# Performance work log

Measured on AMD Instinct MI355X. Metric: run time of the kernel, lower is better.

## Reference

```python
import jax, jax.numpy as jnp
import numpy as np

NUM_HEADS = 16
HEAD_DIM = 64
ROPE_THETA = 10000.0


def _rope_cos_sin(n, dtype):
    # Llama RoPE: inv_freq over even dims, emb = concat(freqs, freqs)
    inv_freq = 1.0 / (ROPE_THETA ** (jnp.arange(0, HEAD_DIM, 2, dtype=jnp.float32) / HEAD_DIM))
    freqs = jnp.arange(n, dtype=jnp.float32)[:, None] * inv_freq[None, :]  # [N, D/2]
    emb = jnp.concatenate([freqs, freqs], axis=-1)  # [N, D]
    return jnp.cos(emb).astype(dtype), jnp.sin(emb).astype(dtype)


def _rotate_half(x):
    x1, x2 = jnp.split(x, 2, axis=-1)
    return jnp.concatenate([-x2, x1], axis=-1)


def setup_inputs() -> dict:
    key = jax.random.key(0)
    ks = jax.random.split(key, 5)
    B, N, H = 2, 2048, 1024
    feature = jax.random.normal(ks[0], (B, N, H), dtype=jnp.float32)
    attention_mask = jnp.ones((B, N), dtype=jnp.int32)
    scale = 0.02
    Wq = jax.random.normal(ks[1], (H, H), dtype=jnp.float32) * scale
    Wk = jax.random.normal(ks[2], (H, H), dtype=jnp.float32) * scale
    Wv = jax.random.normal(ks[3], (H, H), dtype=jnp.float32) * scale
    Wo = jax.random.normal(ks[4], (H, H), dtype=jnp.float32) * scale
    return {"feature": feature, "attention_mask": attention_mask,
            "Wq": Wq, "Wk": Wk, "Wv": Wv, "Wo": Wo}


def reference(feature, attention_mask, Wq, Wk, Wv, Wo):
    B, N, H = feature.shape
    h, d = NUM_HEADS, HEAD_DIM
    scale = d ** -0.5

    def proj(x, W):  # nn.Linear(bias=False): x @ W.T
        y = jnp.einsum('bnh,oh->bno', x, W)
        return y.reshape(B, N, h, d).transpose(0, 2, 1, 3)  # [B,h,N,d]

    q, k, v = proj(feature, Wq), proj(feature, Wk), proj(feature, Wv)

    cos, sin = _rope_cos_sin(N, feature.dtype)  # [N, d]
    cos = cos[None, None]  # [1,1,N,d]
    sin = sin[None, None]
    q = q * cos + _rotate_half(q) * sin
    k = k * cos + _rotate_half(k) * sin

    scores = jnp.einsum('bhqd,bhkd->bhqk', q, k) * scale  # [B,h,N,N]
    mask = (attention_mask != 0)[:, None, None, :]  # [B,1,1,N]
    scores = jnp.where(mask, scores, jnp.float32(-jnp.inf).astype(scores.dtype))
    weights = jax.nn.softmax(scores, axis=-1)

    out = jnp.einsum('bhqk,bhkd->bhqd', weights, v)  # [B,h,N,d]
    out = out.transpose(0, 2, 1, 3).reshape(B, N, H)
    return jnp.einsum('bnh,oh->bno', out, Wo)
```

## Files before the change

### kernel.cpp

```cpp
#include <hip/hip_runtime.h>
#include <hip/hip_bf16.h>

typedef __attribute__((ext_vector_type(4))) float f32x4;
typedef __attribute__((ext_vector_type(8))) short s16x8;
typedef __attribute__((ext_vector_type(4))) short s16x4;

#define BB 2
#define NN 2048
#define HH 1024
#define NHEAD 16
#define HDIM 64

__device__ __forceinline__ short f2bf(float f) {
  union { float f; unsigned u; } v; v.f = f;
  unsigned r = v.u + 0x7fffu + ((v.u >> 16) & 1u);
  return (short)(r >> 16);
}

__device__ __forceinline__ f32x4 zf4() { f32x4 z; z[0]=0.f; z[1]=0.f; z[2]=0.f; z[3]=0.f; return z; }

__device__ __forceinline__ f32x4 mfma16(s16x8 a, s16x8 b, f32x4 c) {
  return __builtin_amdgcn_mfma_f32_16x16x32_bf16(a, b, c, 0, 0, 0);
}

__device__ __forceinline__ s16x4 cvt4(f32x4 v) {
  s16x4 o; o[0]=f2bf(v[0]); o[1]=f2bf(v[1]); o[2]=f2bf(v[2]); o[3]=f2bf(v[3]); return o;
}

__device__ __forceinline__ float vexp2(float x) {
  float r; asm("v_exp_f32 %0, %1" : "=v"(r) : "v"(x)); return r;
}

__device__ __forceinline__ float vrcp(float x) {
  float r; asm("v_rcp_f32 %0, %1" : "=v"(r) : "v"(x)); return r;
}

__device__ __forceinline__ unsigned cvtpk_bf16(float lo, float hi) {
  unsigned r; asm("v_cvt_pk_bf16_f32 %0, %1, %2" : "=v"(r) : "v"(lo), "v"(hi)); return r;
}

__global__ __launch_bounds__(256) void prep_kernel(
    const float* __restrict__ feat, const int* __restrict__ mask,
    const float* __restrict__ wq, const float* __restrict__ wk,
    const float* __restrict__ wv, const float* __restrict__ wo,
    short* __restrict__ fbf, short* __restrict__ wqb, short* __restrict__ wkb,
    short* __restrict__ wvb, short* __restrict__ wob,
    float* __restrict__ cosb, float* __restrict__ sinb,
    float* __restrict__ mbias, int* __restrict__ mseg) {
  const int tid = blockIdx.x * blockDim.x + threadIdx.x;
  const int nth = gridDim.x * blockDim.x;
  const int NF4 = BB*NN*HH/4;
  for (int i = tid; i < NF4; i += nth)
    ((s16x4*)fbf)[i] = cvt4(((const f32x4*)feat)[i]);
  const int NW4 = HH*HH/4;
  for (int i = tid; i < NW4; i += nth) {
    ((s16x4*)wqb)[i] = cvt4(((const f32x4*)wq)[i]);
    ((s16x4*)wkb)[i] = cvt4(((const f32x4*)wk)[i]);
    ((s16x4*)wvb)[i] = cvt4(((const f32x4*)wv)[i]);
    ((s16x4*)wob)[i] = cvt4(((const f32x4*)wo)[i]);
  }
  for (int i = tid; i < NN*32; i += nth) {
    int pos = i >> 5, f = i & 31;
    float inv = __expf(-(float)f * 0.28782313662425572f);
    float ang = (float)pos * inv;
    float s, c;
    sincosf(ang, &s, &c);
    cosb[i] = c; sinb[i] = s;
  }
  for (int i = tid; i < BB*NN; i += nth)
    mbias[i] = mask[i] ? 0.f : -1.0e30f;
  for (int i = tid; i < BB*(NN/64); i += nth) {
    int bb = i / (NN/64), sg = i % (NN/64);
    int any = 0;
    for (int j = 0; j < 64; ++j) any |= (mask[bb*NN + sg*64 + j] == 0);
    mseg[i] = any;
  }
}

__device__ __forceinline__ void gemm128_core(
    const short* __restrict__ A, const short* __restrict__ W,
    int bm, int bn, short* smem, f32x4 acc[4][4]) {
  const int tid = threadIdx.x;
  const int lane = tid & 63, wid = tid >> 6;
  const int wr = wid >> 1, wc = wid & 1;
  const int g = lane >> 4, lr = lane & 15;
  short* At = smem;
  short* Bt = smem + 5120;
#pragma unroll
  for (int i = 0; i < 4; ++i)
#pragma unroll
    for (int j = 0; j < 4; ++j) acc[i][j] = zf4();

  const int srow = tid >> 2;
  const int scol = (tid & 3) * 8;
  const short* Aptr = A + (size_t)(bm*128 + srow) * HH + scol;
  const short* Wptr = W + (size_t)(bn*128 + srow) * HH + scol;

  s16x8 ra0 = *(const s16x8*)(Aptr);
  s16x8 ra1 = *(const s16x8*)(Aptr + 64*HH);
  s16x8 rb0 = *(const s16x8*)(Wptr);
  s16x8 rb1 = *(const s16x8*)(Wptr + 64*HH);

  const int NT = HH / 32;
  for (int t = 0; t < NT; ++t) {
    *(s16x8*)&At[srow*40 + scol]      = ra0;
    *(s16x8*)&At[(srow+64)*40 + scol] = ra1;
    *(s16x8*)&Bt[srow*40 + scol]      = rb0;
    *(s16x8*)&Bt[(srow+64)*40 + scol] = rb1;
    __syncthreads();
    if (t + 1 < NT) {
      const short* ap = Aptr + (t+1)*32;
      const short* wp = Wptr + (t+1)*32;
      ra0 = *(const s16x8*)(ap);
      ra1 = *(const s16x8*)(ap + 64*HH);
      rb0 = *(const s16x8*)(wp);
      rb1 = *(const s16x8*)(wp + 64*HH);
    }
    s16x8 af[4], bf[4];
#pragma unroll
    for (int mf = 0; mf < 4; ++mf)
      af[mf] = *(const s16x8*)&At[(wr*64 + mf*16 + lr)*40 + g*8];
#pragma unroll
    for (int nf = 0; nf < 4; ++nf)
      bf[nf] = *(const s16x8*)&Bt[(wc*64 + nf*16 + lr)*40 + g*8];
#pragma unroll
    for (int mf = 0; mf < 4; ++mf)
#pragma unroll
      for (int nf = 0; nf < 4; ++nf)
        acc[mf][nf] = mfma16(af[mf], bf[nf], acc[mf][nf]);
    __syncthreads();
  }
}

__global__ __launch_bounds__(256) void qkv_kernel(
    const short* __restrict__ fbf, const short* __restrict__ wqb,
    const short* __restrict__ wkb, const short* __restrict__ wvb,
    const float* __restrict__ cosb, const float* __restrict__ sinb,
    short* __restrict__ qb, short* __restrict__ kb, short* __restrict__ vtb) {
  __shared__ short smem[18432];
  const int bm = blockIdx.y, bn = blockIdx.x, z = blockIdx.z;
  const short* W = (z == 0) ? wqb : ((z == 1) ? wkb : wvb);
  f32x4 acc[4][4];
  gemm128_core(fbf, W, bm, bn, smem, acc);

  const int tid = threadIdx.x, lane = tid & 63, wid = tid >> 6;
  const int wr = wid >> 1, wc = wid & 1, g = lane >> 4, lr = lane & 15;
  const int head = bn*2 + wc;
  const int m0 = bm*128 + wr*64;
  const int b = m0 / NN;

  if (z < 2) {
    short* dst = (z == 0) ? qb : kb;
    const float scale = (z == 0) ? 0.18033688011112042f : 1.0f;
#pragma unroll
    for (int mf = 0; mf < 4; ++mf) {
#pragma unroll
      for (int r = 0; r < 4; ++r) {
        int m = m0 + mf*16 + g*4 + r;
        int n = m & (NN - 1);
        float c0 = cosb[n*32 + lr],      s0 = sinb[n*32 + lr];
        float c1 = cosb[n*32 + 16 + lr], s1 = sinb[n*32 + 16 + lr];
        float v0 = acc[mf][0][r], v1 = acc[mf][1][r];
        float v2 = acc[mf][2][r], v3 = acc[mf][3][r];
        float o0 = (v0*c0 - v2*s0) * scale;
        float o1 = (v1*c1 - v3*s1) * scale;
        float o2 = (v2*c0 + v0*s0) * scale;
        float o3 = (v3*c1 + v1*s1) * scale;
        size_t base = ((size_t)(b*NHEAD + head)*NN + n)*HDIM;
        dst[base +  0 + lr] = f2bf(o0);
        dst[base + 16 + lr] = f2bf(o1);
        dst[base + 32 + lr] = f2bf(o2);
        dst[base + 48 + lr] = f2bf(o3);
      }
    }
  } else {
    __syncthreads();
    short* tp = smem + wid*4608;
#pragma unroll
    for (int mf = 0; mf < 4; ++mf)
#pragma unroll
      for (int nf = 0; nf < 4; ++nf)
#pragma unroll
        for (int r = 0; r < 4; ++r)
          tp[(nf*16 + lr)*72 + mf*16 + g*4 + r] = f2bf(acc[mf][nf][r]);
    __syncthreads();
    const int nbase = m0 & (NN - 1);
    size_t vbase = ((size_t)(b*NHEAD + head)*HDIM)*NN;
#pragma unroll
    for (int it = 0; it < 8; ++it) {
      int j  = it*8 + (lane >> 3);
      int ns = (lane & 7)*8;
      s16x8 vv = *(const s16x8*)&tp[j*72 + ns];
      *(s16x8*)&vtb[vbase + (size_t)j*NN + nbase + ns] = vv;
    }
  }
}

__global__ __launch_bounds__(256) void attn_kernel(
    const short* __restrict__ qb, const short* __restrict__ kb,
    const short* __restrict__ vtb, const float* __restrict__ mbias,
    const int* __restrict__ mseg,
    short* __restrict__ attnb) {
  __shared__ short Kt[64*72];
  __shared__ short Vt[64*72];
  __shared__ __align__(16) unsigned Pd[4][16*36];
  const int tid = threadIdx.x, lane = tid & 63, wid = tid >> 6;
  const int g = lane >> 4, lr = lane & 15;
  const int bh = blockIdx.y; const int b = bh >> 4;
  const int q0 = blockIdx.x*64 + wid*16;

  const short* qp = qb + ((size_t)bh*NN + q0 + lr)*HDIM + g*8;
  s16x8 qf0 = *(const s16x8*)(qp);
  s16x8 qf1 = *(const s16x8*)(qp + 32);

  f32x4 acc[4];
#pragma unroll
  for (int i = 0; i < 4; ++i) acc[i] = zf4();
  float mrun = -3.0e38f, lsum = 0.f;

  const int sr = tid >> 2;
  const int sc = (tid & 3) * 16;
  const short* kp = kb + (size_t)bh*NN*HDIM + (size_t)sr*HDIM + sc;
  const short* vp = vtb + ((size_t)bh*HDIM + sr)*NN + sc;
  const float* mb = mbias + b*NN;
  const int* msp = mseg + b*(NN/64);

  s16x8 kr0 = *(const s16x8*)(kp);
  s16x8 kr1 = *(const s16x8*)(kp + 8);
  s16x8 vr0 = *(const s16x8*)(vp);
  s16x8 vr1 = *(const s16x8*)(vp + 8);

  for (int k0 = 0; k0 < NN; k0 += 64) {
    *(s16x8*)&Kt[sr*72 + sc]     = kr0;
    *(s16x8*)&Kt[sr*72 + sc + 8] = kr1;
    *(s16x8*)&Vt[sr*72 + sc]     = vr0;
    *(s16x8*)&Vt[sr*72 + sc + 8] = vr1;
    __syncthreads();
    if (k0 + 64 < NN) {
      kp += 64*HDIM; vp += 64;
      kr0 = *(const s16x8*)(kp);
      kr1 = *(const s16x8*)(kp + 8);
      vr0 = *(const s16x8*)(vp);
      vr1 = *(const s16x8*)(vp + 8);
    }

    f32x4 s[4];
    __builtin_amdgcn_s_setprio(1);
#pragma unroll
    for (int kg = 0; kg < 4; ++kg) {
      s16x8 ka0 = *(const s16x8*)&Kt[(kg*16 + lr)*72 + g*8];
      s16x8 ka1 = *(const s16x8*)&Kt[(kg*16 + lr)*72 + 32 + g*8];
      s[kg] = mfma16(ka1, qf1, mfma16(ka0, qf0, zf4()));
    }
    __builtin_amdgcn_s_setprio(0);

    if (msp[k0 >> 6]) {
#pragma unroll
      for (int kg = 0; kg < 4; ++kg) {
        f32x4 bi = *(const f32x4*)&mb[k0 + kg*16 + g*4];
#pragma unroll
        for (int r = 0; r < 4; ++r) s[kg][r] += bi[r];
      }
    }

    float m0a = fmaxf(fmaxf(s[0][0], s[0][1]), fmaxf(s[0][2], s[0][3]));
    float m1a = fmaxf(fmaxf(s[1][0], s[1][1]), fmaxf(s[1][2], s[1][3]));
    float m2a = fmaxf(fmaxf(s[2][0], s[2][1]), fmaxf(s[2][2], s[2][3]));
    float m3a = fmaxf(fmaxf(s[3][0], s[3][1]), fmaxf(s[3][2], s[3][3]));
    float rmax = fmaxf(fmaxf(m0a, m1a), fmaxf(m2a, m3a));
    rmax = fmaxf(rmax, __shfl_xor(rmax, 16));
    rmax = fmaxf(rmax, __shfl_xor(rmax, 32));

    if (__any(rmax > mrun + 8.f)) {
      float mnew = fmaxf(mrun, rmax);
      float al = vexp2(mrun - mnew);
      mrun = mnew;
      lsum *= al;
      float alr[4];
#pragma unroll
      for (int r = 0; r < 4; ++r)
        alr[r] = __shfl(al, (lane & 48) | (g*4 + r));
#pragma unroll
      for (int db = 0; db < 4; ++db)
#pragma unroll
        for (int r = 0; r < 4; ++r) acc[db][r] *= alr[r];
    }

#pragma unroll
    for (int kg = 0; kg < 4; ++kg) {
      float p0 = vexp2(s[kg][0] - mrun);
      float p1 = vexp2(s[kg][1] - mrun);
      float p2 = vexp2(s[kg][2] - mrun);
      float p3 = vexp2(s[kg][3] - mrun);
      lsum += (p0 + p1) + (p2 + p3);
      unsigned* prow = &Pd[wid][lr*36 + kg*8 + g*2];
      prow[0] = cvtpk_bf16(p0, p1);
      prow[1] = cvtpk_bf16(p2, p3);
    }

    s16x8 pa0 = *(const s16x8*)&Pd[wid][lr*36 + g*4];
    s16x8 pa1 = *(const s16x8*)&Pd[wid][lr*36 + 16 + g*4];
    __builtin_amdgcn_s_setprio(1);
#pragma unroll
    for (int db = 0; db < 4; ++db) {
      s16x8 vb0 = *(const s16x8*)&Vt[(db*16 + lr)*72 + g*8];
      s16x8 vb1 = *(const s16x8*)&Vt[(db*16 + lr)*72 + 32 + g*8];
      acc[db] = mfma16(pa0, vb0, acc[db]);
      acc[db] = mfma16(pa1, vb1, acc[db]);
    }
    __builtin_amdgcn_s_setprio(0);
    __syncthreads();
  }

  lsum += __shfl_xor(lsum, 16);
  lsum += __shfl_xor(lsum, 32);
  float inv = vrcp(lsum);
  float invr[4];
#pragma unroll
  for (int r = 0; r < 4; ++r)
    invr[r] = __shfl(inv, (lane & 48) | (g*4 + r));
#pragma unroll
  for (int r = 0; r < 4; ++r) {
    size_t row = (size_t)(b*NN + q0 + g*4 + r);
#pragma unroll
    for (int db = 0; db < 4; ++db)
      attnb[row*HH + (bh & 15)*64 + db*16 + lr] = f2bf(acc[db][r]*invr[r]);
  }
}

__global__ __launch_bounds__(256) void outproj_kernel(
    const short* __restrict__ attnb, const short* __restrict__ wob,
    float* __restrict__ out) {
  __shared__ short smem[10240];
  const int bm = blockIdx.y, bn = blockIdx.x;
  f32x4 acc[4][4];
  gemm128_core(attnb, wob, bm, bn, smem, acc);
  const int tid = threadIdx.x, lane = tid & 63, wid = tid >> 6;
  const int wr = wid >> 1, wc = wid & 1, g = lane >> 4, lr = lane & 15;
  const int m0 = bm*128 + wr*64;
  const int c0 = bn*128 + wc*64;
#pragma unroll
  for (int mf = 0; mf < 4; ++mf)
#pragma unroll
    for (int r = 0; r < 4; ++r) {
      int m = m0 + mf*16 + g*4 + r;
      float* po = out + (size_t)m*HH + c0;
#pragma unroll
      for (int nf = 0; nf < 4; ++nf)
        po[nf*16 + lr] = acc[mf][nf][r];
    }
}

extern "C" void kernel_launch(void* const* d_in, const int* in_sizes, int n_in,
                              void* d_out, int out_size, void* d_ws, size_t ws_size,
                              hipStream_t stream) {
  const float* feat = (const float*)d_in[0];
  const int*   mask = (const int*)d_in[1];
  const float* wq   = (const float*)d_in[2];
  const float* wk   = (const float*)d_in[3];
  const float* wv   = (const float*)d_in[4];
  const float* wo   = (const float*)d_in[5];
  float* out = (float*)d_out;

  char* ws = (char*)d_ws;
  size_t off = 0;
  short* fbf = (short*)(ws + off); off += (size_t)BB*NN*HH*2;
  short* wqb = (short*)(ws + off); off += (size_t)HH*HH*2;
  short* wkb = (short*)(ws + off); off += (size_t)HH*HH*2;
  short* wvb = (short*)(ws + off); off += (size_t)HH*HH*2;
  short* wob = (short*)(ws + off); off += (size_t)HH*HH*2;
  float* cosb = (float*)(ws + off); off += (size_t)NN*32*4;
  float* sinb = (float*)(ws + off); off += (size_t)NN*32*4;
  float* mbias = (float*)(ws + off); off += (size_t)BB*NN*4;
  int* msegb = (int*)(ws + off); off += (size_t)BB*(NN/64)*4;
  short* qbuf = (short*)(ws + off); off += (size_t)BB*NN*HH*2;
  short* kbuf = (short*)(ws + off); off += (size_t)BB*NN*HH*2;
  short* vtbuf = (short*)(ws + off); off += (size_t)BB*NN*HH*2;
  short* attnb = (short*)(ws + off); off += (size_t)BB*NN*HH*2;

  prep_kernel<<<1024, 256, 0, stream>>>(feat, mask, wq, wk, wv, wo,
                                        fbf, wqb, wkb, wvb, wob, cosb, sinb,
                                        mbias, msegb);
  qkv_kernel<<<dim3(HH/128, BB*NN/128, 3), 256, 0, stream>>>(
      fbf, wqb, wkb, wvb, cosb, sinb, qbuf, kbuf, vtbuf);
  attn_kernel<<<dim3(NN/64, BB*NHEAD), 256, 0, stream>>>(
      qbuf, kbuf, vtbuf, mbias, msegb, attnb);
  outproj_kernel<<<dim3(HH/128, BB*NN/128), 256, 0, stream>>>(attnb, wob, out);
}
```

Baseline: 141.2 us.

## Load K/V fragments directly from global memory and remap blocks for L2 locality

The attention kernel no longer stages K and V tiles through shared memory with block-wide barriers. Each wave now loads its MFMA operand fragments for K and V straight from global memory, which removes the LDS writes and both __syncthreads per iteration. The grid is flattened and remapped so that consecutive blocks interleave heads, which is meant to spread work across XCDs while keeping each head's K/V reuse in cache. Each of the four waves now reads the full K/V tile on its own, so global and L2 traffic goes up, and the software prefetch of the next tile is dropped, which may expose load latency.

```diff
diff --git a/kernel.cpp b/kernel.cpp
--- a/kernel.cpp
+++ b/kernel.cpp
@@ -196,18 +196,19 @@
   }
 }
 
-__global__ __launch_bounds__(256) void attn_kernel(
+__global__ __launch_bounds__(256, 4) void attn_kernel(
     const short* __restrict__ qb, const short* __restrict__ kb,
     const short* __restrict__ vtb, const float* __restrict__ mbias,
     const int* __restrict__ mseg,
     short* __restrict__ attnb) {
-  __shared__ short Kt[64*72];
-  __shared__ short Vt[64*72];
   __shared__ __align__(16) unsigned Pd[4][16*36];
   const int tid = threadIdx.x, lane = tid & 63, wid = tid >> 6;
   const int g = lane >> 4, lr = lane & 15;
-  const int bh = blockIdx.y; const int b = bh >> 4;
-  const int q0 = blockIdx.x*64 + wid*16;
+  const int w = blockIdx.x;
+  const int bh = (w & 7) * 4 + ((w >> 3) >> 5);
+  const int qt = (w >> 3) & 31;
+  const int b = bh >> 4;
+  const int q0 = qt*64 + wid*16;
 
   const short* qp = qb + ((size_t)bh*NN + q0 + lr)*HDIM + g*8;
   s16x8 qf0 = *(const s16x8*)(qp);
@@ -218,40 +219,32 @@
   for (int i = 0; i < 4; ++i) acc[i] = zf4();
   float mrun = -3.0e38f, lsum = 0.f;
 
-  const int sr = tid >> 2;
-  const int sc = (tid & 3) * 16;
-  const short* kp = kb + (size_t)bh*NN*HDIM + (size_t)sr*HDIM + sc;
-  const short* vp = vtb + ((size_t)bh*HDIM + sr)*NN + sc;
+  const short* kbase = kb + (size_t)bh*NN*HDIM + (size_t)lr*HDIM + g*8;
+  const short* vbase = vtb + ((size_t)bh*HDIM + lr)*NN + g*8;
   const float* mb = mbias + b*NN;
   const int* msp = mseg + b*(NN/64);
 
-  s16x8 kr0 = *(const s16x8*)(kp);
-  s16x8 kr1 = *(const s16x8*)(kp + 8);
-  s16x8 vr0 = *(const s16x8*)(vp);
-  s16x8 vr1 = *(const s16x8*)(vp + 8);
-
+#pragma unroll 1
   for (int k0 = 0; k0 < NN; k0 += 64) {
-    *(s16x8*)&Kt[sr*72 + sc]     = kr0;
-    *(s16x8*)&Kt[sr*72 + sc + 8] = kr1;
-    *(s16x8*)&Vt[sr*72 + sc]     = vr0;
-    *(s16x8*)&Vt[sr*72 + sc + 8] = vr1;
-    __syncthreads();
-    if (k0 + 64 < NN) {
-      kp += 64*HDIM; vp += 64;
-      kr0 = *(const s16x8*)(kp);
-      kr1 = *(const s16x8*)(kp + 8);
-      vr0 = *(const s16x8*)(vp);
-      vr1 = *(const s16x8*)(vp + 8);
+    const short* kp = kbase + (size_t)k0*HDIM;
+    s16x8 kf[8];
+#pragma unroll
+    for (int kg = 0; kg < 4; ++kg) {
+      kf[kg*2]   = *(const s16x8*)(kp + kg*16*HDIM);
+      kf[kg*2+1] = *(const s16x8*)(kp + kg*16*HDIM + 32);
+    }
+    s16x8 vv[8];
+#pragma unroll
+    for (int db = 0; db < 4; ++db) {
+      vv[db*2]   = *(const s16x8*)(vbase + (size_t)db*16*NN + k0);
+      vv[db*2+1] = *(const s16x8*)(vbase + (size_t)db*16*NN + k0 + 32);
     }
 
     f32x4 s[4];
     __builtin_amdgcn_s_setprio(1);
 #pragma unroll
-    for (int kg = 0; kg < 4; ++kg) {
-      s16x8 ka0 = *(const s16x8*)&Kt[(kg*16 + lr)*72 + g*8];
-      s16x8 ka1 = *(const s16x8*)&Kt[(kg*16 + lr)*72 + 32 + g*8];
-      s[kg] = mfma16(ka1, qf1, mfma16(ka0, qf0, zf4()));
-    }
+    for (int kg = 0; kg < 4; ++kg)
+      s[kg] = mfma16(kf[kg*2+1], qf1, mfma16(kf[kg*2], qf0, zf4()));
     __builtin_amdgcn_s_setprio(0);
 
     if (msp[k0 >> 6]) {
@@ -303,13 +296,10 @@
     __builtin_amdgcn_s_setprio(1);
 #pragma unroll
     for (int db = 0; db < 4; ++db) {
-      s16x8 vb0 = *(const s16x8*)&Vt[(db*16 + lr)*72 + g*8];
-      s16x8 vb1 = *(const s16x8*)&Vt[(db*16 + lr)*72 + 32 + g*8];
-      acc[db] = mfma16(pa0, vb0, acc[db]);
-      acc[db] = mfma16(pa1, vb1, acc[db]);
+      acc[db] = mfma16(pa0, vv[db*2],   acc[db]);
+      acc[db] = mfma16(pa1, vv[db*2+1], acc[db]);
     }
     __builtin_amdgcn_s_setprio(0);
-    __syncthreads();
   }
 
   lsum += __shfl_xor(lsum, 16);
@@ -383,7 +373,7 @@
                                         mbias, msegb);
   qkv_kernel<<<dim3(HH/128, BB*NN/128, 3), 256, 0, stream>>>(
       fbf, wqb, wkb, wvb, cosb, sinb, qbuf, kbuf, vtbuf);
-  attn_kernel<<<dim3(NN/64, BB*NHEAD), 256, 0, stream>>>(
+  attn_kernel<<<1024, 256, 0, stream>>>(
       qbuf, kbuf, vtbuf, mbias, msegb, attnb);
   outproj_kernel<<<dim3(HH/128, BB*NN/128), 256, 0, stream>>>(attnb, wob, out);
 }
```

After: 298.6 us. 112% more time.

## Stage GEMM tiles with direct global-to-LDS loads into double-buffered shared memory

Applied to the files above, without the earlier changes.

The shared GEMM core used by the QKV and output projections now uses global_load_lds to write A and W tiles straight into LDS, instead of going through registers. Two LDS buffers alternate so the next K-tile loads while the current one is multiplied. The row padding (stride 40) is dropped for a dense stride-32 layout that matches the direct-load write pattern. This removes VGPR staging and one barrier per iteration, at the cost of possible LDS bank conflicts on fragment reads. Correctness depends on the load-to-LDS traffic being complete before the barrier, which is not explicitly waited on inside the loop.

```diff
diff --git a/kernel.cpp b/kernel.cpp
--- a/kernel.cpp
+++ b/kernel.cpp
@@ -37,6 +37,12 @@
 
 __device__ __forceinline__ unsigned cvtpk_bf16(float lo, float hi) {
   unsigned r; asm("v_cvt_pk_bf16_f32 %0, %1, %2" : "=v"(r) : "v"(lo), "v"(hi)); return r;
+}
+
+__device__ __forceinline__ void gload_lds16(const short* g, short* l) {
+  __builtin_amdgcn_global_load_lds(
+      (const __attribute__((address_space(1))) unsigned*)g,
+      (__attribute__((address_space(3))) unsigned*)l, 16, 0, 0);
 }
 
 __global__ __launch_bounds__(256) void prep_kernel(
@@ -84,51 +90,51 @@
   const int lane = tid & 63, wid = tid >> 6;
   const int wr = wid >> 1, wc = wid & 1;
   const int g = lane >> 4, lr = lane & 15;
-  short* At = smem;
-  short* Bt = smem + 5120;
 #pragma unroll
   for (int i = 0; i < 4; ++i)
 #pragma unroll
     for (int j = 0; j < 4; ++j) acc[i][j] = zf4();
 
-  const int srow = tid >> 2;
-  const int scol = (tid & 3) * 8;
-  const short* Aptr = A + (size_t)(bm*128 + srow) * HH + scol;
-  const short* Wptr = W + (size_t)(bn*128 + srow) * HH + scol;
-
-  s16x8 ra0 = *(const s16x8*)(Aptr);
-  s16x8 ra1 = *(const s16x8*)(Aptr + 64*HH);
-  s16x8 rb0 = *(const s16x8*)(Wptr);
-  s16x8 rb1 = *(const s16x8*)(Wptr + 64*HH);
+  const int srow = wid*16 + (lane >> 2);
+  const int scol = (lane & 3) * 8;
+  const short* Abase = A + (size_t)(bm*128 + srow)*HH + scol;
+  const short* Wbase = W + (size_t)(bn*128 + srow)*HH + scol;
+
+  auto stage = [&](int b, int t) {
+    const short* ga = Abase + t*32;
+    const short* gb = Wbase + t*32;
+    short* la = smem + b*8192 + wid*512;
+    short* lb = smem + b*8192 + 4096 + wid*512;
+    gload_lds16(ga,          la);
+    gload_lds16(ga + 64*HH,  la + 2048);
+    gload_lds16(gb,          lb);
+    gload_lds16(gb + 64*HH,  lb + 2048);
+  };
+
+  stage(0, 0);
+  asm volatile("s_waitcnt vmcnt(0)");
+  __syncthreads();
 
   const int NT = HH / 32;
+  int cur = 0;
   for (int t = 0; t < NT; ++t) {
-    *(s16x8*)&At[srow*40 + scol]      = ra0;
-    *(s16x8*)&At[(srow+64)*40 + scol] = ra1;
-    *(s16x8*)&Bt[srow*40 + scol]      = rb0;
-    *(s16x8*)&Bt[(srow+64)*40 + scol] = rb1;
-    __syncthreads();
-    if (t + 1 < NT) {
-      const short* ap = Aptr + (t+1)*32;
-      const short* wp = Wptr + (t+1)*32;
-      ra0 = *(const s16x8*)(ap);
-      ra1 = *(const s16x8*)(ap + 64*HH);
-      rb0 = *(const s16x8*)(wp);
-      rb1 = *(const s16x8*)(wp + 64*HH);
-    }
+    if (t + 1 < NT) stage(cur ^ 1, t + 1);
+    const short* At = smem + cur*8192;
+    const short* Bt = At + 4096;
     s16x8 af[4], bf[4];
 #pragma unroll
     for (int mf = 0; mf < 4; ++mf)
-      af[mf] = *(const s16x8*)&At[(wr*64 + mf*16 + lr)*40 + g*8];
+      af[mf] = *(const s16x8*)&At[(wr*64 + mf*16 + lr)*32 + g*8];
 #pragma unroll
     for (int nf = 0; nf < 4; ++nf)
-      bf[nf] = *(const s16x8*)&Bt[(wc*64 + nf*16 + lr)*40 + g*8];
+      bf[nf] = *(const s16x8*)&Bt[(wc*64 + nf*16 + lr)*32 + g*8];
 #pragma unroll
     for (int mf = 0; mf < 4; ++mf)
 #pragma unroll
       for (int nf = 0; nf < 4; ++nf)
         acc[mf][nf] = mfma16(af[mf], bf[nf], acc[mf][nf]);
     __syncthreads();
+    cur ^= 1;
   }
 }
 
@@ -331,7 +337,7 @@
 __global__ __launch_bounds__(256) void outproj_kernel(
     const short* __restrict__ attnb, const short* __restrict__ wob,
     float* __restrict__ out) {
-  __shared__ short smem[10240];
+  __shared__ short smem[16384];
   const int bm = blockIdx.y, bn = blockIdx.x;
   f32x4 acc[4][4];
   gemm128_core(attnb, wob, bm, bn, smem, acc);
```

Result: faster. 134.6 us (-4.7%).
